# Kernel optimization log

Hardware: AMD Instinct MI355X
Metric: run time of the kernel (lower is better)

The kernel has to match this reference:

```python
import jax, jax.numpy as jnp
import numpy as np

H = 8          # num_heads
D = 64         # head_dim
IN = 512       # input_dim
SCALE = D ** -0.5


def setup_inputs() -> dict:
    key = jax.random.key(0)
    ks = jax.random.split(key, 5)
    b, n = 4, 2048
    inner = H * D
    x = jax.random.normal(ks[0], (b, n, IN), dtype=jnp.float32)
    # nn.Linear weights stored as [out, in]; apply as x @ W.T
    Wq = jax.random.normal(ks[1], (inner, IN), dtype=jnp.float32) * (IN ** -0.5)
    Wkv = jax.random.normal(ks[2], (2 * inner, IN), dtype=jnp.float32) * (IN ** -0.5)
    Wo = jax.random.normal(ks[3], (IN, inner), dtype=jnp.float32) * (inner ** -0.5)
    bo = jax.random.normal(ks[4], (IN,), dtype=jnp.float32) * 0.01
    return {"x": x, "Wq": Wq, "Wkv": Wkv, "Wo": Wo, "bo": bo}


def reference(x, Wq, Wkv, Wo, bo):
    b, n, _ = x.shape
    q = jnp.einsum('bni,oi->bno', x, Wq).reshape(b, n, H, D).transpose(0, 2, 1, 3)
    kv = jnp.einsum('bni,oi->bno', x, Wkv)
    k, v = jnp.split(kv, 2, axis=-1)
    k = k.reshape(b, n, H, D).transpose(0, 2, 1, 3)
    v = v.reshape(b, n, H, D).transpose(0, 2, 1, 3)
    attn = jax.nn.softmax(jnp.einsum('bhnd,bhmd->bhnm', q, k) * SCALE, axis=-1)
    # dropout in eval mode: identity
    out = jnp.einsum('bhnm,bhmd->bhnd', attn, v)
    out = out.transpose(0, 2, 1, 3).reshape(b, n, H * D)
    return jnp.einsum('bno,io->bni', out, Wo) + bo
```

## Files before the change

### kernel.cpp

```cpp
#include <hip/hip_runtime.h>
#include <hip/hip_bf16.h>

#define H_ 8
#define D_ 64
#define IN_ 512
#define B_ 4
#define N_ 2048
#define TOK_ (B_*N_)
#define CLOG2_ 0.18033688011112042f

typedef __attribute__((ext_vector_type(8))) short short8;
typedef __attribute__((ext_vector_type(4))) short bs4;
typedef __attribute__((ext_vector_type(4))) float f32x4;

__device__ __forceinline__ unsigned short f2bf(float f) {
  unsigned int u = __float_as_uint(f);
  u += 0x7FFFu + ((u >> 16) & 1u);
  return (unsigned short)(u >> 16);
}

__device__ __forceinline__ short8 cvt8(const float4 a, const float4 b) {
  union { short8 v; __hip_bfloat162 h[4]; } z;
  z.h[0] = __float22bfloat162_rn(make_float2(a.x, a.y));
  z.h[1] = __float22bfloat162_rn(make_float2(a.z, a.w));
  z.h[2] = __float22bfloat162_rn(make_float2(b.x, b.y));
  z.h[3] = __float22bfloat162_rn(make_float2(b.z, b.w));
  return z.v;
}

__device__ __forceinline__ bs4 pack4(float a, float b, float c, float d) {
  union { bs4 v; __hip_bfloat162 h[2]; } z;
  z.h[0] = __float22bfloat162_rn(make_float2(a, b));
  z.h[1] = __float22bfloat162_rn(make_float2(c, d));
  return z.v;
}

__device__ __forceinline__ short8 assemble_p(bs4 pa, bs4 pb) {
  union { bs4 v; unsigned int w[2]; } A, B;
  A.v = pa; B.v = pb;
  auto s0 = __builtin_amdgcn_permlane32_swap(A.w[0], B.w[0], false, false);
  auto s1 = __builtin_amdgcn_permlane32_swap(A.w[1], B.w[1], false, false);
  auto t0 = __builtin_amdgcn_permlane16_swap(s0[0], s0[1], false, false);
  auto t1 = __builtin_amdgcn_permlane16_swap(s1[0], s1[1], false, false);
  union { short8 v; unsigned int w[4]; } R;
  R.w[0] = t0[0];
  R.w[1] = t1[0];
  R.w[2] = t0[1];
  R.w[3] = t1[1];
  return R.v;
}

__device__ __forceinline__ void gld16(const unsigned short* g, unsigned short* l) {
  __builtin_amdgcn_global_load_lds(
      (const __attribute__((address_space(1))) void*)g,
      (__attribute__((address_space(3))) void*)l, 16, 0, 0);
}

__global__ __launch_bounds__(256) void conv_all_kernel(
    const float* __restrict__ x, const float* __restrict__ Wq,
    const float* __restrict__ Wkv, const float* __restrict__ Wo,
    unsigned short* __restrict__ xbf, unsigned short* __restrict__ wbf,
    unsigned short* __restrict__ wobf)
{
  const int b = blockIdx.x;
  const float* src;
  unsigned short* dst;
  size_t base;
  if (b < 2048)      { src = x;   dst = xbf;             base = (size_t)b * 2048; }
  else if (b < 2176) { src = Wq;  dst = wbf;             base = (size_t)(b - 2048) * 2048; }
  else if (b < 2432) { src = Wkv; dst = wbf + 512 * 512; base = (size_t)(b - 2176) * 2048; }
  else               { src = Wo;  dst = wobf;            base = (size_t)(b - 2432) * 2048; }
  size_t i = base + (size_t)threadIdx.x * 8;
  float4 a = *(const float4*)(src + i);
  float4 c = *(const float4*)(src + i + 4);
  *(short8*)(dst + i) = cvt8(a, c);
}

__global__ __launch_bounds__(256) void qkv_gemm_kernel(
    const unsigned short* __restrict__ xbf, const unsigned short* __restrict__ wbf,
    unsigned short* __restrict__ qws, unsigned short* __restrict__ kws,
    unsigned short* __restrict__ vws)
{
  __shared__ __attribute__((aligned(16))) unsigned short sm[128 * 136];

  const int lid = blockIdx.x + (blockIdx.y << 6);
  const int swz = (lid & 7) * 96 + (lid >> 3);
  const int t0 = (swz / 12) * 128;
  const int c0 = (swz % 12) * 128;
  const int cls = c0 >> 9;

  const int tid = threadIdx.x;
  const int wave = tid >> 6, lane = tid & 63;
  const int quad = lane >> 4, l16 = lane & 15;
  const int wm = wave >> 1, wn = wave & 1;

  const int r_ = tid >> 2;
  const int gc = (tid & 3) ^ (r_ & 3);
  const unsigned short* abase = xbf + (size_t)(t0 + r_) * IN_ + gc * 8;
  const unsigned short* bbase = wbf + (size_t)(c0 + r_) * IN_ + gc * 8;

  auto stage = [&](int k0, int buf) {
    unsigned short* sA = sm + buf * 8192;
    unsigned short* sB = sA + 4096;
    gld16(abase + k0,            sA + tid * 8);
    gld16(abase + 64 * IN_ + k0, sA + 2048 + tid * 8);
    gld16(bbase + k0,            sB + tid * 8);
    gld16(bbase + 64 * IN_ + k0, sB + 2048 + tid * 8);
  };

  f32x4 acc[4][4];
  #pragma unroll
  for (int i = 0; i < 4; i++)
    #pragma unroll
    for (int j = 0; j < 4; j++) acc[i][j] = (f32x4){0.f, 0.f, 0.f, 0.f};

  stage(0, 0);

  for (int kt = 0; kt < 16; kt++) {
    const int cur = kt & 1;
    __syncthreads();
    if (kt + 1 < 16) stage((kt + 1) * 32, cur ^ 1);
    const unsigned short* sA = sm + cur * 8192;
    const unsigned short* sB = sA + 4096;
    const int sw = ((quad ^ (l16 & 3)) << 3);
    short8 af[4], bf[4];
    #pragma unroll
    for (int mi = 0; mi < 4; mi++)
      af[mi] = *(const short8*)&sA[(wm * 64 + mi * 16 + l16) * 32 + sw];
    #pragma unroll
    for (int ni = 0; ni < 4; ni++)
      bf[ni] = *(const short8*)&sB[(wn * 64 + ni * 16 + l16) * 32 + sw];
    #pragma unroll
    for (int mi = 0; mi < 4; mi++)
      #pragma unroll
      for (int ni = 0; ni < 4; ni++)
        acc[mi][ni] = __builtin_amdgcn_mfma_f32_16x16x32_bf16(af[mi], bf[ni], acc[mi][ni], 0, 0, 0);
  }

  __syncthreads();

  if (cls < 2) {
    const float qs = (cls == 0) ? CLOG2_ : 1.0f;
    #pragma unroll
    for (int mi = 0; mi < 4; mi++) {
      const int row0 = wm * 64 + mi * 16 + quad * 4;
      #pragma unroll
      for (int ni = 0; ni < 4; ni++) {
        const int col = wn * 64 + ni * 16 + l16;
        #pragma unroll
        for (int r = 0; r < 4; r++)
          sm[(row0 + r) * 136 + col] = f2bf(acc[mi][ni][r] * qs);
      }
    }
    __syncthreads();
    const int row = tid >> 1, half = tid & 1;
    const int t = t0 + row, bb = t >> 11, nn = t & (N_ - 1);
    const int cw = (c0 & 511) + half * 64;
    const int hh = cw >> 6;
    unsigned short* dst = ((cls == 0) ? qws : kws) +
                          ((size_t)(bb * H_ + hh) * N_ + nn) * D_;
    const unsigned short* srcp = &sm[row * 136 + half * 64];
    #pragma unroll
    for (int j = 0; j < 8; j++)
      *(uint4*)(dst + j * 8) = *(const uint4*)(srcp + j * 8);
  } else {
    #pragma unroll
    for (int mi = 0; mi < 4; mi++) {
      const int tk = wm * 64 + mi * 16 + quad * 4;
      #pragma unroll
      for (int ni = 0; ni < 4; ni++) {
        const int col = wn * 64 + ni * 16 + l16;
        bs4 pk4 = pack4(acc[mi][ni][0], acc[mi][ni][1], acc[mi][ni][2], acc[mi][ni][3]);
        *(bs4*)&sm[col * 136 + tk] = pk4;
      }
    }
    __syncthreads();
    const int col = tid >> 1, half = tid & 1;
    const int cw = (c0 - 1024) + col;
    const int hh = cw >> 6, dd = cw & 63;
    const int bb = t0 >> 11, n0 = (t0 & (N_ - 1)) + half * 64;
    unsigned short* dst = vws + ((size_t)(bb * H_ + hh) * D_ + dd) * N_ + n0;
    const unsigned short* srcp = &sm[col * 136 + half * 64];
    #pragma unroll
    for (int j = 0; j < 8; j++)
      *(uint4*)(dst + j * 8) = *(const uint4*)(srcp + j * 8);
  }
}

__global__ __launch_bounds__(512, 4) void attention_kernel(
    const unsigned short* __restrict__ qws,
    const unsigned short* __restrict__ kws,
    const unsigned short* __restrict__ vws,
    unsigned short* __restrict__ ows)
{
  __shared__ __attribute__((aligned(16))) unsigned short sm[3][8192];
  __shared__ float sml[128];

  const int lid = blockIdx.x + (blockIdx.y << 4);
  const int swz = ((lid & 7) << 6) + (lid >> 3);
  const int q0 = (swz & 15) * 128;
  const int bh = swz >> 4;
  const int tid = threadIdx.x;
  const int wave = tid >> 6, lane = tid & 63;
  const int quad = lane >> 4, l16 = lane & 15;
  const int rbw = wave & 3;
  const int kh = wave >> 2;

  const unsigned short* qbase = qws + (size_t)bh * N_ * D_;
  const unsigned short* kbase = kws + (size_t)bh * N_ * D_;
  const unsigned short* vbase = vws + (size_t)bh * D_ * N_;

  short8 qf[2][2];
  #pragma unroll
  for (int rb = 0; rb < 2; rb++) {
    const int qrow = q0 + rbw * 32 + rb * 16 + l16;
    #pragma unroll
    for (int kc = 0; kc < 2; kc++)
      qf[rb][kc] = *(const short8*)(qbase + (size_t)qrow * D_ + kc * 32 + quad * 8);
  }

  f32x4 ot[2][4];
  f32x4 otl[2];
  #pragma unroll
  for (int rb = 0; rb < 2; rb++) {
    #pragma unroll
    for (int db = 0; db < 4; db++) ot[rb][db] = (f32x4){0.f, 0.f, 0.f, 0.f};
    otl[rb] = (f32x4){0.f, 0.f, 0.f, 0.f};
  }
  const short8 ones8 = {(short)0x3F80, (short)0x3F80, (short)0x3F80, (short)0x3F80,
                        (short)0x3F80, (short)0x3F80, (short)0x3F80, (short)0x3F80};

  const int r_ = tid >> 3;
  const int gc = (tid & 7) ^ (r_ & 7);
  const unsigned short* kst = kbase + (size_t)r_ * D_ + gc * 8;
  const unsigned short* vst = vbase + (size_t)r_ * N_ + gc * 8;

  auto stage = [&](int kt, int buf) {
    const int k0 = kt * 64;
    gld16(kst + (size_t)k0 * D_, &sm[buf][0]    + tid * 8);
    gld16(vst + k0,              &sm[buf][4096] + tid * 8);
  };

  const int NT = N_ / 64;
  stage(0, 0);
  stage(1, 1);

  for (int kt = 0; kt < NT; kt++) {
    if (kt < NT - 1) asm volatile("s_waitcnt vmcnt(2)" ::: "memory");
    else             asm volatile("s_waitcnt vmcnt(0)" ::: "memory");
    __builtin_amdgcn_s_barrier();
    if (kt + 2 < NT) stage(kt + 2, (kt + 2) % 3);

    const unsigned short* Ks = &sm[kt % 3][0];
    const unsigned short* Vs = &sm[kt % 3][4096];

    f32x4 st[2][2];
    #pragma unroll
    for (int rb = 0; rb < 2; rb++)
      #pragma unroll
      for (int nb = 0; nb < 2; nb++) st[rb][nb] = (f32x4){0.f, 0.f, 0.f, 0.f};
    #pragma unroll
    for (int kc = 0; kc < 2; kc++) {
      const int sw = (((kc * 4 + quad) ^ (l16 & 7)) << 3);
      #pragma unroll
      for (int nb = 0; nb < 2; nb++) {
        short8 kf = *(const short8*)&Ks[(kh * 32 + nb * 16 + l16) * 64 + sw];
        st[0][nb] = __builtin_amdgcn_mfma_f32_16x16x32_bf16(kf, qf[0][kc], st[0][nb], 0, 0, 0);
        st[1][nb] = __builtin_amdgcn_mfma_f32_16x16x32_bf16(kf, qf[1][kc], st[1][nb], 0, 0, 0);
      }
    }

    short8 pA[2];
    #pragma unroll
    for (int rb = 0; rb < 2; rb++) {
      bs4 pf[2];
      #pragma unroll
      for (int nb = 0; nb < 2; nb++) {
        float p0 = __builtin_amdgcn_exp2f(st[rb][nb][0]);
        float p1 = __builtin_amdgcn_exp2f(st[rb][nb][1]);
        float p2 = __builtin_amdgcn_exp2f(st[rb][nb][2]);
        float p3 = __builtin_amdgcn_exp2f(st[rb][nb][3]);
        pf[nb] = pack4(p0, p1, p2, p3);
      }
      pA[rb] = assemble_p(pf[0], pf[1]);
    }

    {
      const int slot = (((kh * 4 + quad) ^ (l16 & 7)) << 3);
      short8 vf8[4];
      #pragma unroll
      for (int db = 0; db < 4; db++)
        vf8[db] = *(const short8*)&Vs[(db * 16 + l16) * 64 + slot];
      #pragma unroll
      for (int rb = 0; rb < 2; rb++) {
        #pragma unroll
        for (int db = 0; db < 4; db++)
          ot[rb][db] = __builtin_amdgcn_mfma_f32_16x16x32_bf16(vf8[db], pA[rb], ot[rb][db], 0, 0, 0);
        otl[rb] = __builtin_amdgcn_mfma_f32_16x16x32_bf16(ones8, pA[rb], otl[rb], 0, 0, 0);
      }
    }
  }

  __syncthreads();
  float* Of = (float*)sm;
  if (kh == 1) {
    #pragma unroll
    for (int rb = 0; rb < 2; rb++) {
      const int q = rbw * 32 + rb * 16 + l16;
      #pragma unroll
      for (int db = 0; db < 4; db++) {
        const int slot = (db * 4 + quad) ^ l16;
        *(f32x4*)&Of[q * 64 + slot * 4] = ot[rb][db];
      }
      if (quad == 0) sml[q] = otl[rb][0];
    }
  }
  __syncthreads();
  bs4 pk[2][4];
  if (kh == 0) {
    #pragma unroll
    for (int rb = 0; rb < 2; rb++) {
      const int q = rbw * 32 + rb * 16 + l16;
      const float inv = 1.f / (otl[rb][0] + sml[q]);
      #pragma unroll
      for (int db = 0; db < 4; db++) {
        const int slot = (db * 4 + quad) ^ l16;
        f32x4 p = *(const f32x4*)&Of[q * 64 + slot * 4];
        pk[rb][db] = pack4((ot[rb][db][0] + p[0]) * inv, (ot[rb][db][1] + p[1]) * inv,
                           (ot[rb][db][2] + p[2]) * inv, (ot[rb][db][3] + p[3]) * inv);
      }
    }
  }
  __syncthreads();
  unsigned short* Os = (unsigned short*)sm;
  if (kh == 0) {
    #pragma unroll
    for (int rb = 0; rb < 2; rb++)
      #pragma unroll
      for (int db = 0; db < 4; db++)
        *(bs4*)&Os[(rbw * 32 + rb * 16 + l16) * 72 + db * 16 + quad * 4] = pk[rb][db];
  }
  __syncthreads();
  const int b_ = bh >> 3, h_ = bh & 7;
  const int qloc = tid >> 2, chunk = tid & 3;
  unsigned short* dst = ows + ((size_t)b_ * N_ + q0 + qloc) * (H_ * D_) + h_ * 64 + chunk * 16;
  const unsigned short* srcp = &Os[qloc * 72 + chunk * 16];
  *(uint4*)dst = *(const uint4*)srcp;
  *(uint4*)(dst + 8) = *(const uint4*)(srcp + 8);
}

__global__ __launch_bounds__(256) void out_gemm_kernel(
    const unsigned short* __restrict__ ain, const unsigned short* __restrict__ wobf,
    const float* __restrict__ bo, float* __restrict__ y)
{
  __shared__ __attribute__((aligned(16))) unsigned short sm[12288];

  const int lid = blockIdx.x + (blockIdx.y << 6);
  const int swz = ((lid & 7) << 6) + (lid >> 3);
  const int t0 = (swz >> 3) * 128;
  const int c0 = (swz & 7) * 64;
  const int tid = threadIdx.x;
  const int wave = tid >> 6, lane = tid & 63;
  const int quad = lane >> 4, l16 = lane & 15;

  const int r_ = tid >> 2;
  const int gc = (tid & 3) ^ (r_ & 3);
  const unsigned short* abase = ain  + (size_t)(t0 + r_) * IN_ + gc * 8;
  const unsigned short* bbase = wobf + (size_t)(c0 + r_) * IN_ + gc * 8;

  auto stage = [&](int k0, int buf) {
    unsigned short* sA = sm + buf * 6144;
    unsigned short* sB = sA + 4096;
    gld16(abase + k0,            sA + tid * 8);
    gld16(abase + 64 * IN_ + k0, sA + 2048 + tid * 8);
    gld16(bbase + k0,            sB + tid * 8);
  };

  f32x4 acc[2][4];
  #pragma unroll
  for (int i = 0; i < 2; i++)
    #pragma unroll
    for (int j = 0; j < 4; j++) acc[i][j] = (f32x4){0.f, 0.f, 0.f, 0.f};

  stage(0, 0);

  for (int kt = 0; kt < 16; kt++) {
    const int cur = kt & 1;
    __syncthreads();
    if (kt + 1 < 16) stage((kt + 1) * 32, cur ^ 1);
    const unsigned short* sA = sm + cur * 6144;
    const unsigned short* sB = sA + 4096;
    const int sw = ((quad ^ (l16 & 3)) << 3);
    short8 af[2], bf[4];
    #pragma unroll
    for (int mi = 0; mi < 2; mi++)
      af[mi] = *(const short8*)&sA[(wave * 32 + mi * 16 + l16) * 32 + sw];
    #pragma unroll
    for (int ni = 0; ni < 4; ni++)
      bf[ni] = *(const short8*)&sB[(ni * 16 + l16) * 32 + sw];
    #pragma unroll
    for (int mi = 0; mi < 2; mi++)
      #pragma unroll
      for (int ni = 0; ni < 4; ni++)
        acc[mi][ni] = __builtin_amdgcn_mfma_f32_16x16x32_bf16(af[mi], bf[ni], acc[mi][ni], 0, 0, 0);
  }

  #pragma unroll
  for (int mi = 0; mi < 2; mi++) {
    const int t = t0 + wave * 32 + mi * 16 + quad * 4;
    #pragma unroll
    for (int ni = 0; ni < 4; ni++) {
      const int c = c0 + ni * 16 + l16;
      const float bias = bo[c];
      float* dst = y + (size_t)t * IN_ + c;
      dst[0]        = acc[mi][ni][0] + bias;
      dst[IN_]      = acc[mi][ni][1] + bias;
      dst[2 * IN_]  = acc[mi][ni][2] + bias;
      dst[3 * IN_]  = acc[mi][ni][3] + bias;
    }
  }
}

extern "C" void kernel_launch(void* const* d_in, const int* in_sizes, int n_in,
                              void* d_out, int out_size, void* d_ws, size_t ws_size,
                              hipStream_t stream) {
  const float* x   = (const float*)d_in[0];
  const float* Wq  = (const float*)d_in[1];
  const float* Wkv = (const float*)d_in[2];
  const float* Wo  = (const float*)d_in[3];
  const float* bo  = (const float*)d_in[4];
  float* out = (float*)d_out;

  unsigned short* qws  = (unsigned short*)d_ws;
  unsigned short* kws  = qws + (size_t)TOK_ * 512;
  unsigned short* vws  = kws + (size_t)TOK_ * 512;
  unsigned short* ows  = vws + (size_t)TOK_ * 512;
  unsigned short* wbf  = ows + (size_t)TOK_ * 512;
  unsigned short* wobf = wbf + (size_t)1536 * 512;
  unsigned short* xbf  = ows;

  conv_all_kernel<<<dim3(2560), 256, 0, stream>>>(x, Wq, Wkv, Wo, xbf, wbf, wobf);
  qkv_gemm_kernel<<<dim3(TOK_ / 128, 1536 / 128), 256, 0, stream>>>(xbf, wbf, qws, kws, vws);
  attention_kernel<<<dim3(N_ / 128, B_ * H_), 512, 0, stream>>>(qws, kws, vws, ows);
  out_gemm_kernel<<<dim3(TOK_ / 128, 512 / 64), 256, 0, stream>>>(ows, wobf, bo, out);
}
```

Baseline: 152.0 us.

## Halve attention block to 4 waves, each handling 64 query rows

The attention kernel now launches 256 threads (4 waves) instead of 512. Each wave covers 64 query rows across 4 row blocks, up from 32, so every K/V fragment read from shared memory feeds twice as many MFMAs. Each thread now issues two async loads per K and V tile, and the wait count is adjusted to match. The cost is more accumulator registers per thread and fewer waves per CU, which may reduce latency hiding.

```diff
diff --git a/kernel.cpp b/kernel.cpp
--- a/kernel.cpp
+++ b/kernel.cpp
@@ -187,7 +187,7 @@
   }
 }
 
-__global__ __launch_bounds__(512, 4) void attention_kernel(
+__global__ __launch_bounds__(256, 3) void attention_kernel(
     const unsigned short* __restrict__ qws,
     const unsigned short* __restrict__ kws,
     const unsigned short* __restrict__ vws,
@@ -203,26 +203,26 @@
   const int tid = threadIdx.x;
   const int wave = tid >> 6, lane = tid & 63;
   const int quad = lane >> 4, l16 = lane & 15;
-  const int rbw = wave & 3;
-  const int kh = wave >> 2;
+  const int rbw = wave & 1;
+  const int kh = wave >> 1;
 
   const unsigned short* qbase = qws + (size_t)bh * N_ * D_;
   const unsigned short* kbase = kws + (size_t)bh * N_ * D_;
   const unsigned short* vbase = vws + (size_t)bh * D_ * N_;
 
-  short8 qf[2][2];
-  #pragma unroll
-  for (int rb = 0; rb < 2; rb++) {
-    const int qrow = q0 + rbw * 32 + rb * 16 + l16;
+  short8 qf[4][2];
+  #pragma unroll
+  for (int rb = 0; rb < 4; rb++) {
+    const int qrow = q0 + rbw * 64 + rb * 16 + l16;
     #pragma unroll
     for (int kc = 0; kc < 2; kc++)
       qf[rb][kc] = *(const short8*)(qbase + (size_t)qrow * D_ + kc * 32 + quad * 8);
   }
 
-  f32x4 ot[2][4];
-  f32x4 otl[2];
-  #pragma unroll
-  for (int rb = 0; rb < 2; rb++) {
+  f32x4 ot[4][4];
+  f32x4 otl[4];
+  #pragma unroll
+  for (int rb = 0; rb < 4; rb++) {
     #pragma unroll
     for (int db = 0; db < 4; db++) ot[rb][db] = (f32x4){0.f, 0.f, 0.f, 0.f};
     otl[rb] = (f32x4){0.f, 0.f, 0.f, 0.f};
@@ -237,8 +237,10 @@
 
   auto stage = [&](int kt, int buf) {
     const int k0 = kt * 64;
-    gld16(kst + (size_t)k0 * D_, &sm[buf][0]    + tid * 8);
-    gld16(vst + k0,              &sm[buf][4096] + tid * 8);
+    gld16(kst + (size_t)k0 * D_,              &sm[buf][0]    + tid * 8);
+    gld16(kst + (size_t)(k0 + 32) * D_,       &sm[buf][2048] + tid * 8);
+    gld16(vst + k0,                           &sm[buf][4096] + tid * 8);
+    gld16(vst + k0 + 32 * N_,                 &sm[buf][6144] + tid * 8);
   };
 
   const int NT = N_ / 64;
@@ -246,7 +248,7 @@
   stage(1, 1);
 
   for (int kt = 0; kt < NT; kt++) {
-    if (kt < NT - 1) asm volatile("s_waitcnt vmcnt(2)" ::: "memory");
+    if (kt < NT - 1) asm volatile("s_waitcnt vmcnt(4)" ::: "memory");
     else             asm volatile("s_waitcnt vmcnt(0)" ::: "memory");
     __builtin_amdgcn_s_barrier();
     if (kt + 2 < NT) stage(kt + 2, (kt + 2) % 3);
@@ -254,32 +256,33 @@
     const unsigned short* Ks = &sm[kt % 3][0];
     const unsigned short* Vs = &sm[kt % 3][4096];
 
-    f32x4 st[2][2];
-    #pragma unroll
-    for (int rb = 0; rb < 2; rb++)
-      #pragma unroll
-      for (int nb = 0; nb < 2; nb++) st[rb][nb] = (f32x4){0.f, 0.f, 0.f, 0.f};
+    short8 kf[2][2];
     #pragma unroll
     for (int kc = 0; kc < 2; kc++) {
       const int sw = (((kc * 4 + quad) ^ (l16 & 7)) << 3);
       #pragma unroll
+      for (int nb = 0; nb < 2; nb++)
+        kf[kc][nb] = *(const short8*)&Ks[(kh * 32 + nb * 16 + l16) * 64 + sw];
+    }
+
+    short8 pA[4];
+    #pragma unroll
+    for (int rb = 0; rb < 4; rb++) {
+      f32x4 st[2];
+      st[0] = (f32x4){0.f, 0.f, 0.f, 0.f};
+      st[1] = (f32x4){0.f, 0.f, 0.f, 0.f};
+      #pragma unroll
+      for (int kc = 0; kc < 2; kc++) {
+        st[0] = __builtin_amdgcn_mfma_f32_16x16x32_bf16(kf[kc][0], qf[rb][kc], st[0], 0, 0, 0);
+        st[1] = __builtin_amdgcn_mfma_f32_16x16x32_bf16(kf[kc][1], qf[rb][kc], st[1], 0, 0, 0);
+      }
+      bs4 pf[2];
+      #pragma unroll
       for (int nb = 0; nb < 2; nb++) {
-        short8 kf = *(const short8*)&Ks[(kh * 32 + nb * 16 + l16) * 64 + sw];
-        st[0][nb] = __builtin_amdgcn_mfma_f32_16x16x32_bf16(kf, qf[0][kc], st[0][nb], 0, 0, 0);
-        st[1][nb] = __builtin_amdgcn_mfma_f32_16x16x32_bf16(kf, qf[1][kc], st[1][nb], 0, 0, 0);
-      }
-    }
-
-    short8 pA[2];
-    #pragma unroll
-    for (int rb = 0; rb < 2; rb++) {
-      bs4 pf[2];
-      #pragma unroll
-      for (int nb = 0; nb < 2; nb++) {
-        float p0 = __builtin_amdgcn_exp2f(st[rb][nb][0]);
-        float p1 = __builtin_amdgcn_exp2f(st[rb][nb][1]);
-        float p2 = __builtin_amdgcn_exp2f(st[rb][nb][2]);
-        float p3 = __builtin_amdgcn_exp2f(st[rb][nb][3]);
+        float p0 = __builtin_amdgcn_exp2f(st[nb][0]);
+        float p1 = __builtin_amdgcn_exp2f(st[nb][1]);
+        float p2 = __builtin_amdgcn_exp2f(st[nb][2]);
+        float p3 = __builtin_amdgcn_exp2f(st[nb][3]);
         pf[nb] = pack4(p0, p1, p2, p3);
       }
       pA[rb] = assemble_p(pf[0], pf[1]);
@@ -292,7 +295,7 @@
       for (int db = 0; db < 4; db++)
         vf8[db] = *(const short8*)&Vs[(db * 16 + l16) * 64 + slot];
       #pragma unroll
-      for (int rb = 0; rb < 2; rb++) {
+      for (int rb = 0; rb < 4; rb++) {
         #pragma unroll
         for (int db = 0; db < 4; db++)
           ot[rb][db] = __builtin_amdgcn_mfma_f32_16x16x32_bf16(vf8[db], pA[rb], ot[rb][db], 0, 0, 0);
@@ -305,8 +308,8 @@
   float* Of = (float*)sm;
   if (kh == 1) {
     #pragma unroll
-    for (int rb = 0; rb < 2; rb++) {
-      const int q = rbw * 32 + rb * 16 + l16;
+    for (int rb = 0; rb < 4; rb++) {
+      const int q = rbw * 64 + rb * 16 + l16;
       #pragma unroll
       for (int db = 0; db < 4; db++) {
         const int slot = (db * 4 + quad) ^ l16;
@@ -316,11 +319,11 @@
     }
   }
   __syncthreads();
-  bs4 pk[2][4];
+  bs4 pk[4][4];
   if (kh == 0) {
     #pragma unroll
-    for (int rb = 0; rb < 2; rb++) {
-      const int q = rbw * 32 + rb * 16 + l16;
+    for (int rb = 0; rb < 4; rb++) {
+      const int q = rbw * 64 + rb * 16 + l16;
       const float inv = 1.f / (otl[rb][0] + sml[q]);
       #pragma unroll
       for (int db = 0; db < 4; db++) {
@@ -335,18 +338,19 @@
   unsigned short* Os = (unsigned short*)sm;
   if (kh == 0) {
     #pragma unroll
-    for (int rb = 0; rb < 2; rb++)
+    for (int rb = 0; rb < 4; rb++)
       #pragma unroll
       for (int db = 0; db < 4; db++)
-        *(bs4*)&Os[(rbw * 32 + rb * 16 + l16) * 72 + db * 16 + quad * 4] = pk[rb][db];
+        *(bs4*)&Os[(rbw * 64 + rb * 16 + l16) * 72 + db * 16 + quad * 4] = pk[rb][db];
   }
   __syncthreads();
   const int b_ = bh >> 3, h_ = bh & 7;
-  const int qloc = tid >> 2, chunk = tid & 3;
-  unsigned short* dst = ows + ((size_t)b_ * N_ + q0 + qloc) * (H_ * D_) + h_ * 64 + chunk * 16;
-  const unsigned short* srcp = &Os[qloc * 72 + chunk * 16];
-  *(uint4*)dst = *(const uint4*)srcp;
-  *(uint4*)(dst + 8) = *(const uint4*)(srcp + 8);
+  const int qloc = tid >> 1, chunk = tid & 1;
+  unsigned short* dst = ows + ((size_t)b_ * N_ + q0 + qloc) * (H_ * D_) + h_ * 64 + chunk * 32;
+  const unsigned short* srcp = &Os[qloc * 72 + chunk * 32];
+  #pragma unroll
+  for (int j = 0; j < 4; j++)
+    *(uint4*)(dst + j * 8) = *(const uint4*)(srcp + j * 8);
 }
 
 __global__ __launch_bounds__(256) void out_gemm_kernel(
@@ -441,6 +445,6 @@
 
   conv_all_kernel<<<dim3(2560), 256, 0, stream>>>(x, Wq, Wkv, Wo, xbf, wbf, wobf);
   qkv_gemm_kernel<<<dim3(TOK_ / 128, 1536 / 128), 256, 0, stream>>>(xbf, wbf, qws, kws, vws);
-  attention_kernel<<<dim3(N_ / 128, B_ * H_), 512, 0, stream>>>(qws, kws, vws, ows);
+  attention_kernel<<<dim3(N_ / 128, B_ * H_), 256, 0, stream>>>(qws, kws, vws, ows);
   out_gemm_kernel<<<dim3(TOK_ / 128, 512 / 64), 256, 0, stream>>>(ows, wobf, bo, out);
 }
```

Result: no change. 154.9 us (+1.9%).

## Shrink attention blocks to 64 queries with double-buffered K/V staging

Applied to the files above, without the earlier changes.

Halves the attention block to 256 threads covering 64 query rows, doubling the grid. It replaces the triple-buffered K/V pipeline with a double buffer that issues four 16-byte loads per thread per tile and waits for all outstanding loads each iteration. The QK^T MFMAs are reordered so K fragments are loaded once and the S tile for each row block is computed and exponentiated right away, which may lower register pressure. The aim is higher occupancy and less LDS per block. The cost is shallower prefetch and twice the K/V global traffic per query row.

```diff
diff --git a/kernel.cpp b/kernel.cpp
--- a/kernel.cpp
+++ b/kernel.cpp
@@ -187,24 +187,24 @@
   }
 }
 
-__global__ __launch_bounds__(512, 4) void attention_kernel(
+__global__ __launch_bounds__(256, 4) void attention_kernel(
     const unsigned short* __restrict__ qws,
     const unsigned short* __restrict__ kws,
     const unsigned short* __restrict__ vws,
     unsigned short* __restrict__ ows)
 {
-  __shared__ __attribute__((aligned(16))) unsigned short sm[3][8192];
-  __shared__ float sml[128];
-
-  const int lid = blockIdx.x + (blockIdx.y << 4);
-  const int swz = ((lid & 7) << 6) + (lid >> 3);
-  const int q0 = (swz & 15) * 128;
-  const int bh = swz >> 4;
+  __shared__ __attribute__((aligned(16))) unsigned short sm[2][8192];
+  __shared__ float sml[64];
+
+  const int lid = blockIdx.x + (blockIdx.y << 5);
+  const int swz = ((lid & 7) << 7) + (lid >> 3);
+  const int q0 = (swz & 31) * 64;
+  const int bh = swz >> 5;
   const int tid = threadIdx.x;
   const int wave = tid >> 6, lane = tid & 63;
   const int quad = lane >> 4, l16 = lane & 15;
-  const int rbw = wave & 3;
-  const int kh = wave >> 2;
+  const int rbw = wave & 1;
+  const int kh = wave >> 1;
 
   const unsigned short* qbase = qws + (size_t)bh * N_ * D_;
   const unsigned short* kbase = kws + (size_t)bh * N_ * D_;
@@ -237,49 +237,50 @@
 
   auto stage = [&](int kt, int buf) {
     const int k0 = kt * 64;
-    gld16(kst + (size_t)k0 * D_, &sm[buf][0]    + tid * 8);
-    gld16(vst + k0,              &sm[buf][4096] + tid * 8);
+    gld16(kst + (size_t)k0 * D_,              &sm[buf][0]    + tid * 8);
+    gld16(kst + (size_t)(k0 + 32) * D_,       &sm[buf][2048] + tid * 8);
+    gld16(vst + k0,                           &sm[buf][4096] + tid * 8);
+    gld16(vst + k0 + 32 * N_,                 &sm[buf][6144] + tid * 8);
   };
 
   const int NT = N_ / 64;
   stage(0, 0);
-  stage(1, 1);
 
   for (int kt = 0; kt < NT; kt++) {
-    if (kt < NT - 1) asm volatile("s_waitcnt vmcnt(2)" ::: "memory");
-    else             asm volatile("s_waitcnt vmcnt(0)" ::: "memory");
+    asm volatile("s_waitcnt vmcnt(0)" ::: "memory");
     __builtin_amdgcn_s_barrier();
-    if (kt + 2 < NT) stage(kt + 2, (kt + 2) % 3);
-
-    const unsigned short* Ks = &sm[kt % 3][0];
-    const unsigned short* Vs = &sm[kt % 3][4096];
-
-    f32x4 st[2][2];
-    #pragma unroll
-    for (int rb = 0; rb < 2; rb++)
-      #pragma unroll
-      for (int nb = 0; nb < 2; nb++) st[rb][nb] = (f32x4){0.f, 0.f, 0.f, 0.f};
+    if (kt + 1 < NT) stage(kt + 1, (kt + 1) & 1);
+
+    const unsigned short* Ks = &sm[kt & 1][0];
+    const unsigned short* Vs = &sm[kt & 1][4096];
+
+    short8 kf[2][2];
     #pragma unroll
     for (int kc = 0; kc < 2; kc++) {
       const int sw = (((kc * 4 + quad) ^ (l16 & 7)) << 3);
       #pragma unroll
+      for (int nb = 0; nb < 2; nb++)
+        kf[kc][nb] = *(const short8*)&Ks[(kh * 32 + nb * 16 + l16) * 64 + sw];
+    }
+
+    short8 pA[2];
+    #pragma unroll
+    for (int rb = 0; rb < 2; rb++) {
+      f32x4 st[2];
+      st[0] = (f32x4){0.f, 0.f, 0.f, 0.f};
+      st[1] = (f32x4){0.f, 0.f, 0.f, 0.f};
+      #pragma unroll
+      for (int kc = 0; kc < 2; kc++) {
+        st[0] = __builtin_amdgcn_mfma_f32_16x16x32_bf16(kf[kc][0], qf[rb][kc], st[0], 0, 0, 0);
+        st[1] = __builtin_amdgcn_mfma_f32_16x16x32_bf16(kf[kc][1], qf[rb][kc], st[1], 0, 0, 0);
+      }
+      bs4 pf[2];
+      #pragma unroll
       for (int nb = 0; nb < 2; nb++) {
-        short8 kf = *(const short8*)&Ks[(kh * 32 + nb * 16 + l16) * 64 + sw];
-        st[0][nb] = __builtin_amdgcn_mfma_f32_16x16x32_bf16(kf, qf[0][kc], st[0][nb], 0, 0, 0);
-        st[1][nb] = __builtin_amdgcn_mfma_f32_16x16x32_bf16(kf, qf[1][kc], st[1][nb], 0, 0, 0);
-      }
-    }
-
-    short8 pA[2];
-    #pragma unroll
-    for (int rb = 0; rb < 2; rb++) {
-      bs4 pf[2];
-      #pragma unroll
-      for (int nb = 0; nb < 2; nb++) {
-        float p0 = __builtin_amdgcn_exp2f(st[rb][nb][0]);
-        float p1 = __builtin_amdgcn_exp2f(st[rb][nb][1]);
-        float p2 = __builtin_amdgcn_exp2f(st[rb][nb][2]);
-        float p3 = __builtin_amdgcn_exp2f(st[rb][nb][3]);
+        float p0 = __builtin_amdgcn_exp2f(st[nb][0]);
+        float p1 = __builtin_amdgcn_exp2f(st[nb][1]);
+        float p2 = __builtin_amdgcn_exp2f(st[nb][2]);
+        float p3 = __builtin_amdgcn_exp2f(st[nb][3]);
         pf[nb] = pack4(p0, p1, p2, p3);
       }
       pA[rb] = assemble_p(pf[0], pf[1]);
@@ -441,6 +442,6 @@
 
   conv_all_kernel<<<dim3(2560), 256, 0, stream>>>(x, Wq, Wkv, Wo, xbf, wbf, wobf);
   qkv_gemm_kernel<<<dim3(TOK_ / 128, 1536 / 128), 256, 0, stream>>>(xbf, wbf, qws, kws, vws);
-  attention_kernel<<<dim3(N_ / 128, B_ * H_), 512, 0, stream>>>(qws, kws, vws, ows);
+  attention_kernel<<<dim3(N_ / 64, B_ * H_), 256, 0, stream>>>(qws, kws, vws, ows);
   out_gemm_kernel<<<dim3(TOK_ / 128, 512 / 64), 256, 0, stream>>>(ows, wobf, bo, out);
 }
```

Result: slower. 157.7 us (+3.8%).
